# Optimization experiments

Hardware: AMD Instinct MI355X
Metric: run time of the kernel (lower is better)

## Reference

```python
import jax, jax.numpy as jnp
import numpy as np

TWO_PI = 6.283185307179586


def setup_inputs() -> dict:
    key = jax.random.key(0)
    k1, k2, k3, k4, k5, k6 = jax.random.split(key, 6)
    B, T, D = 2, 8192, 1024
    x = jax.random.normal(k1, (B, T, D), dtype=jnp.float32)
    # nn.Linear weights are [out, in]; init with small scale like torch default
    s = 1.0 / np.sqrt(D)
    Wk = jax.random.uniform(k2, (D, D), jnp.float32, -s, s)
    Wv = jax.random.uniform(k3, (D, D), jnp.float32, -s, s)
    Wo = jax.random.uniform(k4, (D, D), jnp.float32, -s, s)
    # random phasor frequencies in [0, 2*pi)
    freqs = jax.random.uniform(k5, (D,), jnp.float32, 0.0, TWO_PI)
    return {"x": x, "Wk": Wk, "Wv": Wv, "Wo": Wo, "freqs": freqs}


def reference(x, Wk, Wv, Wo, freqs):
    B, T, C = x.shape
    # k projection is computed in the original forward but never used downstream
    k_real = x @ Wk.T  # [B,T,D] (dead value, kept for fidelity)
    v_real = x @ Wv.T  # [B,T,D]
    v = v_real.astype(jnp.complex64)
    # rotors: per-position unit phasors exp(i * t * freqs), shape [T, D]
    t = jnp.arange(T, dtype=jnp.float32)
    rotors = jnp.exp(1j * (t[:, None] * freqs[None, :])).astype(jnp.complex64)
    # bind each value with its rotor and accumulate causally (O(N) memory trace)
    memory_trace = jnp.cumsum(v * rotors[None, :, :], axis=1)  # [B,T,D] complex64
    # retrieve by unbinding with the conjugate rotor; take the real component
    retrieved = jnp.real(memory_trace * jnp.conj(rotors)[None, :, :])  # [B,T,D]
    return retrieved @ Wo.T
```

## Files before the change

### kernel.cpp

```cpp
#include <hip/hip_runtime.h>
#include <hip/hip_bf16.h>


#define B_  2
#define T_  8192
#define D_  1024
#define BT_ 16384
#define CS_ 64
#define NCHUNK_ 128

typedef __attribute__((ext_vector_type(4))) float f32x4;
typedef __attribute__((ext_vector_type(8))) short bf16x8;

static __device__ inline unsigned short f2bf(float f) {
    union { float f; unsigned int u; } a;
    a.f = f;
    unsigned int u = a.u;
    return (unsigned short)((u + 0x7FFFu + ((u >> 16) & 1u)) >> 16);
}
static __device__ inline float bf2f(unsigned short h) {
    union { unsigned int u; float f; } a;
    a.u = ((unsigned int)h) << 16;
    return a.f;
}

__global__ __launch_bounds__(256) void cast_f32_bf16(const float* __restrict__ in,
                                                     unsigned short* __restrict__ out, int n4) {
    int i = blockIdx.x * 256 + threadIdx.x;
    if (i < n4) {
        float4 v = ((const float4*)in)[i];
        ushort4 o;
        o.x = f2bf(v.x); o.y = f2bf(v.y); o.z = f2bf(v.z); o.w = f2bf(v.w);
        ((ushort4*)out)[i] = o;
    }
}

template <bool BF16OUT>
__global__ __launch_bounds__(256) void gemm_bt(const short* __restrict__ A,
                                               const short* __restrict__ Bm,
                                               void* __restrict__ Cout,
                                               int M, int N, int K) {
    __shared__ short lds[8192];
    const int lane = threadIdx.x & 63;
    const int wave = threadIdx.x >> 6;
    const int wr = wave >> 1, wc = wave & 1;
    const int bm = blockIdx.y * 128, bn = blockIdx.x * 128;

    const int r0 = lane >> 2;
    const int cb = lane & 3;

    const int m_base = wr * 64 + (lane & 15);
    const int n_base = wc * 64 + (lane & 15);
    const int k_off = (lane >> 4) * 8;

    f32x4 acc[4][4] = {};

    for (int k0 = 0; k0 < K; k0 += 32) {
#pragma unroll
        for (int cc = 0; cc < 2; ++cc) {
            const int chunk = wave * 2 + cc;
            const int row = chunk * 16 + r0;
            const short* ga = A + (size_t)(bm + row) * K + k0 + cb * 8;
            const short* gb = Bm + (size_t)(bn + row) * K + k0 + cb * 8;
            __builtin_amdgcn_global_load_lds(
                (const __attribute__((address_space(1))) void*)ga,
                (__attribute__((address_space(3))) void*)&lds[chunk * 512], 16, 0, 0);
            __builtin_amdgcn_global_load_lds(
                (const __attribute__((address_space(1))) void*)gb,
                (__attribute__((address_space(3))) void*)&lds[4096 + chunk * 512], 16, 0, 0);
        }
        __syncthreads();
        bf16x8 a[4], b[4];
#pragma unroll
        for (int i = 0; i < 4; ++i)
            a[i] = *(const bf16x8*)&lds[(m_base + i * 16) * 32 + k_off];
#pragma unroll
        for (int j = 0; j < 4; ++j)
            b[j] = *(const bf16x8*)&lds[4096 + (n_base + j * 16) * 32 + k_off];
#pragma unroll
        for (int i = 0; i < 4; ++i)
#pragma unroll
            for (int j = 0; j < 4; ++j)
                acc[i][j] = __builtin_amdgcn_mfma_f32_16x16x32_bf16(a[i], b[j], acc[i][j], 0, 0, 0);
        __syncthreads();
    }

    const int row0 = (lane >> 4) * 4;
#pragma unroll
    for (int i = 0; i < 4; ++i) {
#pragma unroll
        for (int j = 0; j < 4; ++j) {
            const int col = bn + wc * 64 + j * 16 + (lane & 15);
#pragma unroll
            for (int r = 0; r < 4; ++r) {
                const size_t row = bm + wr * 64 + i * 16 + row0 + r;
                if constexpr (BF16OUT)
                    ((unsigned short*)Cout)[row * N + col] = f2bf(acc[i][j][r]);
                else
                    ((float*)Cout)[row * N + col] = acc[i][j][r];
            }
        }
    }
}

__global__ __launch_bounds__(256) void scan_pass1(const unsigned short* __restrict__ v,
                                                  const float* __restrict__ freqs,
                                                  float* __restrict__ csum) {
    const int d = blockIdx.x * 256 + threadIdx.x;
    const int chunk = blockIdx.y;
    const int b = blockIdx.z;
    const float f = freqs[d];
    const int t0 = chunk * CS_;
    float s, c, sf, cf;
    sincosf((float)t0 * f, &s, &c);
    sincosf(f, &sf, &cf);
    float ar = 0.f, ai = 0.f;
    const unsigned short* vp = v + ((size_t)b * T_ + t0) * D_ + d;
    for (int t = 0; t < CS_; ++t) {
        float w = bf2f(*vp); vp += D_;
        ar = fmaf(w, c, ar); ai = fmaf(w, s, ai);
        float c2 = c * cf - s * sf;
        float s2 = s * cf + c * sf;
        c = c2; s = s2;
    }
    const size_t idx = (((size_t)b * NCHUNK_ + chunk) * D_ + d) * 2;
    csum[idx] = ar; csum[idx + 1] = ai;
}

__global__ __launch_bounds__(256) void scan_pass2(float* __restrict__ csum) {
    const int g = blockIdx.x * 256 + threadIdx.x;
    const int b = g / D_;
    const int d = g % D_;
    float2* cs = (float2*)csum;
    const size_t base = (size_t)b * NCHUNK_ * D_ + d;
    float pr = 0.f, pi = 0.f;
    for (int cc = 0; cc < NCHUNK_; cc += 16) {
        float2 buf[16];
#pragma unroll
        for (int k = 0; k < 16; ++k) buf[k] = cs[base + (size_t)(cc + k) * D_];
#pragma unroll
        for (int k = 0; k < 16; ++k) {
            float r = buf[k].x, im = buf[k].y;
            buf[k] = make_float2(pr, pi);
            pr += r; pi += im;
        }
#pragma unroll
        for (int k = 0; k < 16; ++k) cs[base + (size_t)(cc + k) * D_] = buf[k];
    }
}

__global__ __launch_bounds__(256) void scan_pass3(const unsigned short* __restrict__ v,
                                                  const float* __restrict__ freqs,
                                                  const float* __restrict__ csum,
                                                  unsigned short* __restrict__ ret) {
    const int d = blockIdx.x * 256 + threadIdx.x;
    const int chunk = blockIdx.y;
    const int b = blockIdx.z;
    const float f = freqs[d];
    const size_t cidx = (((size_t)b * NCHUNK_ + chunk) * D_ + d) * 2;
    float ar = csum[cidx], ai = csum[cidx + 1];
    const int t0 = chunk * CS_;
    float s, c, sf, cf;
    sincosf((float)t0 * f, &s, &c);
    sincosf(f, &sf, &cf);
    const unsigned short* vp = v + ((size_t)b * T_ + t0) * D_ + d;
    unsigned short* rp = ret + ((size_t)b * T_ + t0) * D_ + d;
    for (int t = 0; t < CS_; ++t) {
        float w = bf2f(*vp); vp += D_;
        ar = fmaf(w, c, ar); ai = fmaf(w, s, ai);
        *rp = f2bf(ar * c + ai * s);
        rp += D_;
        float c2 = c * cf - s * sf;
        float s2 = s * cf + c * sf;
        c = c2; s = s2;
    }
}

extern "C" void kernel_launch(void* const* d_in, const int* in_sizes, int n_in,
                              void* d_out, int out_size, void* d_ws, size_t ws_size,
                              hipStream_t stream) {
    const float* x     = (const float*)d_in[0];
    const float* Wv    = (const float*)d_in[2];
    const float* Wo    = (const float*)d_in[3];
    const float* freqs = (const float*)d_in[4];
    float* out = (float*)d_out;

    char* ws = (char*)d_ws;
    unsigned short* x_bf  = (unsigned short*)ws;
    unsigned short* Wv_bf = (unsigned short*)(ws + 33554432);
    unsigned short* Wo_bf = (unsigned short*)(ws + 35651584);
    unsigned short* ret   = (unsigned short*)(ws + 37748736);
    float*          csum  = (float*)(ws + 71303168);
    unsigned short* v_bf = (unsigned short*)d_out;

    cast_f32_bf16<<<(BT_ * D_ / 4 + 255) / 256, 256, 0, stream>>>(x, x_bf, BT_ * D_ / 4);
    cast_f32_bf16<<<(D_ * D_ / 4 + 255) / 256, 256, 0, stream>>>(Wv, Wv_bf, D_ * D_ / 4);
    cast_f32_bf16<<<(D_ * D_ / 4 + 255) / 256, 256, 0, stream>>>(Wo, Wo_bf, D_ * D_ / 4);

    gemm_bt<true><<<dim3(D_ / 128, BT_ / 128), 256, 0, stream>>>(
        (const short*)x_bf, (const short*)Wv_bf, (void*)v_bf, BT_, D_, D_);

    dim3 sgrid(D_ / 256, NCHUNK_, B_);
    scan_pass1<<<sgrid, 256, 0, stream>>>(v_bf, freqs, csum);
    scan_pass2<<<(B_ * D_) / 256, 256, 0, stream>>>(csum);
    scan_pass3<<<sgrid, 256, 0, stream>>>(v_bf, freqs, csum, ret);

    gemm_bt<false><<<dim3(D_ / 128, BT_ / 128), 256, 0, stream>>>(
        (const short*)ret, (const short*)Wo_bf, (void*)out, BT_, D_, D_);
}
```

Baseline: 279.0 us.

## Fuse cast kernels, remap GEMM blocks per XCD, vectorize scan passes

```diff
diff --git a/kernel.cpp b/kernel.cpp
--- a/kernel.cpp
+++ b/kernel.cpp
@@ -24,15 +24,25 @@
     return a.f;
 }
 
-__global__ __launch_bounds__(256) void cast_f32_bf16(const float* __restrict__ in,
-                                                     unsigned short* __restrict__ out, int n4) {
+__global__ __launch_bounds__(256) void cast_all(const float* __restrict__ x,
+                                                const float* __restrict__ Wv,
+                                                const float* __restrict__ Wo,
+                                                unsigned short* __restrict__ xb,
+                                                unsigned short* __restrict__ wvb,
+                                                unsigned short* __restrict__ wob) {
+    const int nx = BT_ * D_ / 4;
+    const int nw = D_ * D_ / 4;
     int i = blockIdx.x * 256 + threadIdx.x;
-    if (i < n4) {
-        float4 v = ((const float4*)in)[i];
-        ushort4 o;
-        o.x = f2bf(v.x); o.y = f2bf(v.y); o.z = f2bf(v.z); o.w = f2bf(v.w);
-        ((ushort4*)out)[i] = o;
-    }
+    const float4* src;
+    unsigned short* dst;
+    int j;
+    if (i < nx)            { src = (const float4*)x;  dst = xb;  j = i; }
+    else if (i < nx + nw)  { src = (const float4*)Wv; dst = wvb; j = i - nx; }
+    else                   { src = (const float4*)Wo; dst = wob; j = i - nx - nw; }
+    float4 v = src[j];
+    ushort4 o;
+    o.x = f2bf(v.x); o.y = f2bf(v.y); o.z = f2bf(v.z); o.w = f2bf(v.w);
+    ((ushort4*)dst)[j] = o;
 }
 
 template <bool BF16OUT>
@@ -44,7 +54,13 @@
     const int lane = threadIdx.x & 63;
     const int wave = threadIdx.x >> 6;
     const int wr = wave >> 1, wc = wave & 1;
-    const int bm = blockIdx.y * 128, bn = blockIdx.x * 128;
+
+    const int nb = N >> 7;
+    const int id = blockIdx.x;
+    const int xcd = id & 7;
+    const int slot = id >> 3;
+    const int bn = (slot % nb) * 128;
+    const int bm = (xcd * ((M >> 7) >> 3) + slot / nb) * 128;
 
     const int r0 = lane >> 2;
     const int cb = lane & 3;
@@ -106,25 +122,30 @@
 __global__ __launch_bounds__(256) void scan_pass1(const unsigned short* __restrict__ v,
                                                   const float* __restrict__ freqs,
                                                   float* __restrict__ csum) {
-    const int d = blockIdx.x * 256 + threadIdx.x;
+    const int d0 = (blockIdx.x * 256 + threadIdx.x) * 2;
     const int chunk = blockIdx.y;
     const int b = blockIdx.z;
-    const float f = freqs[d];
+    const float2 f2 = *(const float2*)(freqs + d0);
     const int t0 = chunk * CS_;
-    float s, c, sf, cf;
-    sincosf((float)t0 * f, &s, &c);
-    sincosf(f, &sf, &cf);
-    float ar = 0.f, ai = 0.f;
-    const unsigned short* vp = v + ((size_t)b * T_ + t0) * D_ + d;
+    float s0, c0, s1, c1, sf0, cf0, sf1, cf1;
+    sincosf((float)t0 * f2.x, &s0, &c0);
+    sincosf((float)t0 * f2.y, &s1, &c1);
+    sincosf(f2.x, &sf0, &cf0);
+    sincosf(f2.y, &sf1, &cf1);
+    float ar0 = 0.f, ai0 = 0.f, ar1 = 0.f, ai1 = 0.f;
+    const unsigned int* vp = (const unsigned int*)(v + ((size_t)b * T_ + t0) * D_ + d0);
     for (int t = 0; t < CS_; ++t) {
-        float w = bf2f(*vp); vp += D_;
-        ar = fmaf(w, c, ar); ai = fmaf(w, s, ai);
-        float c2 = c * cf - s * sf;
-        float s2 = s * cf + c * sf;
-        c = c2; s = s2;
-    }
-    const size_t idx = (((size_t)b * NCHUNK_ + chunk) * D_ + d) * 2;
-    csum[idx] = ar; csum[idx + 1] = ai;
+        unsigned int w2 = *vp; vp += D_ / 2;
+        float w0 = bf2f((unsigned short)w2);
+        float w1 = bf2f((unsigned short)(w2 >> 16));
+        ar0 = fmaf(w0, c0, ar0); ai0 = fmaf(w0, s0, ai0);
+        ar1 = fmaf(w1, c1, ar1); ai1 = fmaf(w1, s1, ai1);
+        float nc0 = c0 * cf0 - s0 * sf0, ns0 = s0 * cf0 + c0 * sf0;
+        float nc1 = c1 * cf1 - s1 * sf1, ns1 = s1 * cf1 + c1 * sf1;
+        c0 = nc0; s0 = ns0; c1 = nc1; s1 = ns1;
+    }
+    float4 o; o.x = ar0; o.y = ai0; o.z = ar1; o.w = ai1;
+    *(float4*)(csum + (((size_t)b * NCHUNK_ + chunk) * D_ + d0) * 2) = o;
 }
 
 __global__ __launch_bounds__(256) void scan_pass2(float* __restrict__ csum) {
@@ -153,26 +174,33 @@
                                                   const float* __restrict__ freqs,
                                                   const float* __restrict__ csum,
                                                   unsigned short* __restrict__ ret) {
-    const int d = blockIdx.x * 256 + threadIdx.x;
+    const int d0 = (blockIdx.x * 256 + threadIdx.x) * 2;
     const int chunk = blockIdx.y;
     const int b = blockIdx.z;
-    const float f = freqs[d];
-    const size_t cidx = (((size_t)b * NCHUNK_ + chunk) * D_ + d) * 2;
-    float ar = csum[cidx], ai = csum[cidx + 1];
+    const float2 f2 = *(const float2*)(freqs + d0);
+    const float4 cs4 = *(const float4*)(csum + (((size_t)b * NCHUNK_ + chunk) * D_ + d0) * 2);
+    float ar0 = cs4.x, ai0 = cs4.y, ar1 = cs4.z, ai1 = cs4.w;
     const int t0 = chunk * CS_;
-    float s, c, sf, cf;
-    sincosf((float)t0 * f, &s, &c);
-    sincosf(f, &sf, &cf);
-    const unsigned short* vp = v + ((size_t)b * T_ + t0) * D_ + d;
-    unsigned short* rp = ret + ((size_t)b * T_ + t0) * D_ + d;
+    float s0, c0, s1, c1, sf0, cf0, sf1, cf1;
+    sincosf((float)t0 * f2.x, &s0, &c0);
+    sincosf((float)t0 * f2.y, &s1, &c1);
+    sincosf(f2.x, &sf0, &cf0);
+    sincosf(f2.y, &sf1, &cf1);
+    const unsigned int* vp = (const unsigned int*)(v + ((size_t)b * T_ + t0) * D_ + d0);
+    unsigned int* rp = (unsigned int*)(ret + ((size_t)b * T_ + t0) * D_ + d0);
     for (int t = 0; t < CS_; ++t) {
-        float w = bf2f(*vp); vp += D_;
-        ar = fmaf(w, c, ar); ai = fmaf(w, s, ai);
-        *rp = f2bf(ar * c + ai * s);
-        rp += D_;
-        float c2 = c * cf - s * sf;
-        float s2 = s * cf + c * sf;
-        c = c2; s = s2;
+        unsigned int w2 = *vp; vp += D_ / 2;
+        float w0 = bf2f((unsigned short)w2);
+        float w1 = bf2f((unsigned short)(w2 >> 16));
+        ar0 = fmaf(w0, c0, ar0); ai0 = fmaf(w0, s0, ai0);
+        ar1 = fmaf(w1, c1, ar1); ai1 = fmaf(w1, s1, ai1);
+        float o0 = ar0 * c0 + ai0 * s0;
+        float o1 = ar1 * c1 + ai1 * s1;
+        *rp = (unsigned int)f2bf(o0) | ((unsigned int)f2bf(o1) << 16);
+        rp += D_ / 2;
+        float nc0 = c0 * cf0 - s0 * sf0, ns0 = s0 * cf0 + c0 * sf0;
+        float nc1 = c1 * cf1 - s1 * sf1, ns1 = s1 * cf1 + c1 * sf1;
+        c0 = nc0; s0 = ns0; c1 = nc1; s1 = ns1;
     }
 }
 
@@ -193,18 +221,17 @@
     float*          csum  = (float*)(ws + 71303168);
     unsigned short* v_bf = (unsigned short*)d_out;
 
-    cast_f32_bf16<<<(BT_ * D_ / 4 + 255) / 256, 256, 0, stream>>>(x, x_bf, BT_ * D_ / 4);
-    cast_f32_bf16<<<(D_ * D_ / 4 + 255) / 256, 256, 0, stream>>>(Wv, Wv_bf, D_ * D_ / 4);
-    cast_f32_bf16<<<(D_ * D_ / 4 + 255) / 256, 256, 0, stream>>>(Wo, Wo_bf, D_ * D_ / 4);
-
-    gemm_bt<true><<<dim3(D_ / 128, BT_ / 128), 256, 0, stream>>>(
+    cast_all<<<(BT_ * D_ / 4 + 2 * D_ * D_ / 4) / 256, 256, 0, stream>>>(
+        x, Wv, Wo, x_bf, Wv_bf, Wo_bf);
+
+    gemm_bt<true><<<(BT_ / 128) * (D_ / 128), 256, 0, stream>>>(
         (const short*)x_bf, (const short*)Wv_bf, (void*)v_bf, BT_, D_, D_);
 
-    dim3 sgrid(D_ / 256, NCHUNK_, B_);
+    dim3 sgrid(D_ / 512, NCHUNK_, B_);
     scan_pass1<<<sgrid, 256, 0, stream>>>(v_bf, freqs, csum);
     scan_pass2<<<(B_ * D_) / 256, 256, 0, stream>>>(csum);
     scan_pass3<<<sgrid, 256, 0, stream>>>(v_bf, freqs, csum, ret);
 
-    gemm_bt<false><<<dim3(D_ / 128, BT_ / 128), 256, 0, stream>>>(
+    gemm_bt<false><<<(BT_ / 128) * (D_ / 128), 256, 0, stream>>>(
         (const short*)ret, (const short*)Wo_bf, (void*)out, BT_, D_, D_);
 }
```

Result: faster. 263.4 us (-5.6%).
